# Optimization experiments

Measured on AMD Instinct MI355X. Metric: run time of the kernel, lower is better.

## Reference

```python
import jax, jax.numpy as jnp
import numpy as np
import math

VOCAB = 128
READ_DIM = 128
LOGIT_SCALE = 1.0 / 16.0
NUM_FF = 6
CARRY_DIM = 896
D_MODEL = CARRY_DIM + READ_DIM


def ste_sign(x):
    # forward of the STE sign: +-1, zero -> +1
    return jnp.where(x >= 0, 1.0, -1.0).astype(x.dtype)


def ste_round(x):
    return jnp.round(x)


def setup_inputs() -> dict:
    key = jax.random.key(0)
    k_tok, k_init, k_emb, k_ff, k_head, k_thr = jax.random.split(key, 6)
    tokens = jax.random.randint(k_tok, (64, 512), 0, VOCAB, dtype=jnp.int64) if jax.config.read('jax_enable_x64') else jax.random.randint(k_tok, (64, 512), 0, VOCAB, dtype=jnp.int32)
    initial_lat = jax.random.uniform(k_init, (D_MODEL,), minval=-1.0, maxval=1.0)
    embed_lat = jax.random.uniform(k_emb, (VOCAB, READ_DIM), minval=-1.0, maxval=1.0)
    ff_lat = jax.random.uniform(k_ff, (NUM_FF, D_MODEL, D_MODEL), minval=-1.0, maxval=1.0)
    head_lat = jax.random.uniform(k_head, (READ_DIM, VOCAB), minval=-1.0, maxval=1.0)
    ff_thresh_lat = jax.random.uniform(k_thr, (NUM_FF, D_MODEL), minval=-2.0, maxval=2.0)
    return {
        'tokens': tokens,
        'initial_lat': initial_lat,
        'embed_lat': embed_lat,
        'ff_lat': ff_lat,
        'head_lat': head_lat,
        'ff_thresh_lat': ff_thresh_lat,
    }


def reference(tokens, initial_lat, embed_lat, ff_lat, head_lat, ff_thresh_lat):
    B, T = tokens.shape
    num_ff = ff_lat.shape[0]
    d_model = initial_lat.shape[0]
    carry_dim = d_model - READ_DIM
    act_scale = math.sqrt(d_model)

    initial = ste_sign(initial_lat)          # [d_model]
    embed = ste_sign(embed_lat)              # [VOCAB, read_dim]
    ff = ste_sign(ff_lat)                    # [num_ff, d_model, d_model]
    head = ste_sign(head_lat)                # [read_dim, VOCAB]
    thr = ste_round(ff_thresh_lat)           # [num_ff, d_model]

    x0 = jnp.broadcast_to(initial[None, :], (B, d_model))

    def step(x, tok_t):
        # tok_t: [B]
        h = x
        for i in range(num_ff):
            pre = h @ ff[i]                  # [B, d_model]
            h = ste_sign((pre - thr[i]) / act_scale)
        carry = h[:, :carry_dim]
        read = h[:, carry_dim:]
        logits = read @ head * LOGIT_SCALE   # [B, VOCAB]
        logp = jax.nn.log_softmax(logits, axis=-1)
        loss_t = -jnp.mean(jnp.take_along_axis(logp, tok_t[:, None], axis=1))
        x_new = jnp.concatenate([carry, embed[tok_t]], axis=1)
        return x_new, loss_t

    _, losses = jax.lax.scan(step, x0, tokens.T)  # scan over T
    return jnp.mean(losses)
```

## Files before the change

### kernel.cpp

```cpp
#include <hip/hip_runtime.h>
#include <stdint.h>

typedef unsigned long long u64;
typedef uint32_t u32;

#define VOCAB 128
#define RD 128
#define DM 1024
#define NFF 6
#define BATCH 64
#define TSTEPS 512
#define NLOC 3
#define THR 256

#define OFF_EB    786432
#define OFF_HB    788480
#define OFF_LOSS  790528
#define OFF_XBUF  791040
#define OFF_MBUF  799232
#define OFF_FA    807424
#define OFF_FB    807680

__device__ __forceinline__ void wait_ge(const u32* f, u32 target) {
    while (__hip_atomic_load(f, __ATOMIC_ACQUIRE, __HIP_MEMORY_SCOPE_AGENT) < target)
        __builtin_amdgcn_s_sleep(1);
}

__global__ void pack_ff(const float* __restrict__ ff, u64* __restrict__ ffb) {
    int wid  = blockIdx.x * (blockDim.x >> 6) + (threadIdx.x >> 6);
    int lane = threadIdx.x & 63;
    int jt = wid & 15;
    int w  = (wid >> 4) & 15;
    int i  = wid >> 8;
    int j  = jt * 64 + lane;
    const float* src = ff + ((size_t)(i * DM) + w * 64) * DM + j;
    u64 word = 0;
#pragma unroll
    for (int b = 0; b < 64; ++b) {
        float v = src[(size_t)b * DM];
        word |= (u64)(v < 0.0f) << b;
    }
    ffb[((i * 16 + w) << 10) + j] = word;
}

__global__ void pack_small(const float* __restrict__ emb, const float* __restrict__ head,
                           u64* __restrict__ eb, u64* __restrict__ hb) {
    int tid = threadIdx.x;
    if (tid < 128) {
        int v = tid;
        for (int wd = 0; wd < 2; ++wd) {
            u64 word = 0;
            for (int l = 0; l < 64; ++l)
                word |= (u64)(emb[v * RD + wd * 64 + l] < 0.0f) << l;
            eb[v * 2 + wd] = word;
        }
    } else {
        int v = tid - 128;
        for (int wd = 0; wd < 2; ++wd) {
            u64 word = 0;
            for (int l = 0; l < 64; ++l)
                word |= (u64)(head[(wd * 64 + l) * VOCAB + v] < 0.0f) << l;
            hb[v * 2 + wd] = word;
        }
    }
}

#define PASS(P, L, EMIT) do {                                                   \
    const ulonglong2* hp_ = (const ulonglong2*)hx[P];                           \
    int a0_ = 0, a1_ = 0, a2_ = 0, a3_ = 0;                                     \
    _Pragma("unroll")                                                           \
    for (int q_ = 0; q_ < 8; ++q_) {                                            \
        ulonglong2 hv_ = hp_[q_];                   \
        a0_ += __popcll(hv_.x ^ fr[L][0][2*q_]) + __popcll(hv_.y ^ fr[L][0][2*q_+1]); \
        a1_ += __popcll(hv_.x ^ fr[L][1][2*q_]) + __popcll(hv_.y ^ fr[L][1][2*q_+1]); \
        a2_ += __popcll(hv_.x ^ fr[L][2][2*q_]) + __popcll(hv_.y ^ fr[L][2][2*q_+1]); \
        a3_ += __popcll(hv_.x ^ fr[L][3][2*q_]) + __popcll(hv_.y ^ fr[L][3][2*q_+1]); \
    }                                                                           \
    u64 m0_ = __ballot(a0_ >= cthr[L][0]);                                      \
    u64 m1_ = __ballot(a1_ >= cthr[L][1]);                                      \
    u64 m2_ = __ballot(a2_ >= cthr[L][2]);                                      \
    u64 m3_ = __ballot(a3_ >= cthr[L][3]);                                      \
    EMIT;                                                                       \
    __syncthreads();                                                            \
} while (0)

__global__ void
__attribute__((amdgpu_flat_work_group_size(256, 256), amdgpu_waves_per_eu(1, 1)))
brnn_pipe(const int* __restrict__ tokens,
          const float* __restrict__ initial_lat,
          const float* __restrict__ thr_lat,
          const u64* __restrict__ ffb,
          const u64* __restrict__ eb,
          const u64* __restrict__ hb,
          u64* __restrict__ xbuf, u64* __restrict__ mbuf,
          u32* __restrict__ fA, u32* __restrict__ fB,
          double* __restrict__ losses)
{
    const int blk  = blockIdx.x;
    const int role = blk >> 5;
    const int g    = blk & 31;
    const int tid  = threadIdx.x;
    const int lane = tid & 63;
    const int wv   = tid >> 6;

    __shared__ __align__(16) u64 hx[2][16];
    __shared__ u64 hbL[2 * VOCAB];

    const int lbase = role * NLOC;

    u64 fr[NLOC][4][16];
#pragma unroll
    for (int l = 0; l < NLOC; ++l)
#pragma unroll
        for (int c = 0; c < 4; ++c)
#pragma unroll
            for (int w = 0; w < 16; ++w)
                fr[l][c][w] = ffb[(((lbase + l) * 16 + w) << 10) + c * THR + tid];

    int cthr[NLOC][4];
#pragma unroll
    for (int l = 0; l < NLOC; ++l)
#pragma unroll
        for (int c = 0; c < 4; ++c) {
            int th = (int)rintf(thr_lat[(lbase + l) * DM + c * THR + tid]);
            cthr[l][c] = ((DM - th) >> 1) + 1;
        }

    if (role == 1 && tid < 2 * VOCAB) hbL[tid] = hb[tid];

    double lacc0 = 0.0, lacc1 = 0.0;
    const int r0 = 2 * g;

    if (role == 0) {
        for (int t = 0; t < TSTEPS; ++t) {
#pragma unroll
            for (int ri = 0; ri < 2; ++ri) {
                const int r = r0 + ri;
                if (t == 0) {
#pragma unroll
                    for (int c = 0; c < 4; ++c) {
                        u64 m = __ballot(initial_lat[c * THR + tid] < 0.0f);
                        if (lane == 0) hx[0][c * 4 + wv] = m;
                    }
                } else {
                    wait_ge(&fB[r], (u32)t);
                    if (wv == 0 && lane < 16) hx[0][lane] = xbuf[r * 16 + lane];
                }
                __syncthreads();
                PASS(0, 0, if (lane == 0) { hx[1][wv] = m0_; hx[1][4 + wv] = m1_;
                                            hx[1][8 + wv] = m2_; hx[1][12 + wv] = m3_; });
                PASS(1, 1, if (lane == 0) { hx[0][wv] = m0_; hx[0][4 + wv] = m1_;
                                            hx[0][8 + wv] = m2_; hx[0][12 + wv] = m3_; });
                PASS(0, 2, if (lane == 0) { mbuf[r * 16 + wv] = m0_;
                                            mbuf[r * 16 + 4 + wv] = m1_;
                                            mbuf[r * 16 + 8 + wv] = m2_;
                                            mbuf[r * 16 + 12 + wv] = m3_; });
                if (tid == 0)
                    __hip_atomic_store(&fA[r], (u32)(t + 1), __ATOMIC_RELEASE,
                                       __HIP_MEMORY_SCOPE_AGENT);
            }
        }
    } else {
        for (int t = 0; t < TSTEPS; ++t) {
#pragma unroll
            for (int ri = 0; ri < 2; ++ri) {
                const int r = r0 + ri;
                wait_ge(&fA[r], (u32)(t + 1));
                const int tok = tokens[r * TSTEPS + t];
                u64 enew = 0;
                if (wv == 0 && lane < 2) enew = eb[tok * 2 + lane];
                if (wv == 0 && lane < 16) hx[0][lane] = mbuf[r * 16 + lane];
                __syncthreads();
                PASS(0, 0, if (lane == 0) { hx[1][wv] = m0_; hx[1][4 + wv] = m1_;
                                            hx[1][8 + wv] = m2_; hx[1][12 + wv] = m3_; });
                PASS(1, 1, if (lane == 0) { hx[0][wv] = m0_; hx[0][4 + wv] = m1_;
                                            hx[0][8 + wv] = m2_; hx[0][12 + wv] = m3_; });
                PASS(0, 2, if (lane == 0) {
                        hx[1][wv] = m0_;      hx[1][4 + wv] = m1_;
                        hx[1][8 + wv] = m2_;  hx[1][12 + wv] = m3_;
                        xbuf[r * 16 + wv] = m0_;
                        xbuf[r * 16 + 4 + wv] = m1_;
                        xbuf[r * 16 + 8 + wv] = m2_;
                        if (wv < 2) xbuf[r * 16 + 12 + wv] = m3_; });
                if (wv == 0) {
                    u64 ra = hx[1][14], rb = hx[1][15];
                    u64 h0a = hbL[lane * 2 + 0],        h0b = hbL[lane * 2 + 1];
                    u64 h1a = hbL[(lane + 64) * 2 + 0], h1b = hbL[(lane + 64) * 2 + 1];
                    int d0 = 128 - 2 * (__popcll(ra ^ h0a) + __popcll(rb ^ h0b));
                    int d1 = 128 - 2 * (__popcll(ra ^ h1a) + __popcll(rb ^ h1b));
                    float l0 = (float)d0 * (1.0f / 16.0f);
                    float l1 = (float)d1 * (1.0f / 16.0f);
                    float mx = fmaxf(l0, l1);
#pragma unroll
                    for (int s = 32; s >= 1; s >>= 1) mx = fmaxf(mx, __shfl_xor(mx, s));
                    float se = __expf(l0 - mx) + __expf(l1 - mx);
#pragma unroll
                    for (int s = 32; s >= 1; s >>= 1) se += __shfl_xor(se, s);
                    int   tl   = tok & 63;
                    float la   = __shfl(l0, tl);
                    float lb_  = __shfl(l1, tl);
                    float ltok = (tok >> 6) ? lb_ : la;
                    double dl = (double)(mx + __logf(se) - ltok);
                    if (ri == 0) lacc0 += dl; else lacc1 += dl;
                    if (lane < 2) xbuf[r * 16 + 14 + lane] = enew;
                }
                __syncthreads();
                if (tid == 0)
                    __hip_atomic_store(&fB[r], (u32)(t + 1), __ATOMIC_RELEASE,
                                       __HIP_MEMORY_SCOPE_AGENT);
            }
        }
        if (tid == 0) { losses[r0] = lacc0; losses[r0 + 1] = lacc1; }
    }
}

__global__ void reduce_loss(const double* __restrict__ losses, float* __restrict__ out) {
    int lane = threadIdx.x;
    double v = losses[lane];
#pragma unroll
    for (int s = 32; s >= 1; s >>= 1) v += __shfl_down(v, s);
    if (lane == 0) out[0] = (float)(v * (1.0 / ((double)BATCH * (double)TSTEPS)));
}

extern "C" void kernel_launch(void* const* d_in, const int* in_sizes, int n_in,
                              void* d_out, int out_size, void* d_ws, size_t ws_size,
                              hipStream_t stream) {
    const int*   tokens  = (const int*)d_in[0];
    const float* initial = (const float*)d_in[1];
    const float* embed   = (const float*)d_in[2];
    const float* ff      = (const float*)d_in[3];
    const float* head    = (const float*)d_in[4];
    const float* thrl    = (const float*)d_in[5];

    char* ws = (char*)d_ws;
    u64*    ffb    = (u64*)ws;
    u64*    eb     = (u64*)(ws + OFF_EB);
    u64*    hb     = (u64*)(ws + OFF_HB);
    double* losses = (double*)(ws + OFF_LOSS);
    u64*    xbuf   = (u64*)(ws + OFF_XBUF);
    u64*    mbuf   = (u64*)(ws + OFF_MBUF);
    u32*    fAf    = (u32*)(ws + OFF_FA);
    u32*    fBf    = (u32*)(ws + OFF_FB);

    hipMemsetAsync(ws + OFF_FA, 0, 512, stream);

    pack_ff<<<384, 256, 0, stream>>>(ff, ffb);
    pack_small<<<1, 256, 0, stream>>>(embed, head, eb, hb);
    brnn_pipe<<<BATCH, THR, 0, stream>>>(tokens, initial, thrl, ffb, eb, hb,
                                         xbuf, mbuf, fAf, fBf, losses);
    reduce_loss<<<1, 64, 0, stream>>>(losses, (float*)d_out);
}
```

Baseline: 6.477 ms.

## Double block threads and move third layer's weights into LDS

Each pipeline block now runs 512 threads, so each thread owns 2 output columns per layer instead of 4. The first two layers' packed weights stay in registers and the third layer's weights are staged in shared memory and read during its pass. The aim is to cut the serial popcount work per thread along the recurrence's critical path by spreading it over more waves. The cost is extra LDS traffic in the third pass, more barrier participants, and a changed mapping of ballot words to the hx/mbuf/xbuf layout.

```diff
diff --git a/kernel.cpp b/kernel.cpp
--- a/kernel.cpp
+++ b/kernel.cpp
@@ -11,7 +11,7 @@
 #define BATCH 64
 #define TSTEPS 512
 #define NLOC 3
-#define THR 256
+#define THR 512
 
 #define OFF_EB    786432
 #define OFF_HB    788480
@@ -65,27 +65,40 @@
     }
 }
 
-#define PASS(P, L, EMIT) do {                                                   \
+#define REG_PASS(P, L, EMIT) do {                                               \
     const ulonglong2* hp_ = (const ulonglong2*)hx[P];                           \
-    int a0_ = 0, a1_ = 0, a2_ = 0, a3_ = 0;                                     \
+    int a0_ = 0, a1_ = 0;                                                       \
     _Pragma("unroll")                                                           \
     for (int q_ = 0; q_ < 8; ++q_) {                                            \
         ulonglong2 hv_ = hp_[q_];                   \
         a0_ += __popcll(hv_.x ^ fr[L][0][2*q_]) + __popcll(hv_.y ^ fr[L][0][2*q_+1]); \
         a1_ += __popcll(hv_.x ^ fr[L][1][2*q_]) + __popcll(hv_.y ^ fr[L][1][2*q_+1]); \
-        a2_ += __popcll(hv_.x ^ fr[L][2][2*q_]) + __popcll(hv_.y ^ fr[L][2][2*q_+1]); \
-        a3_ += __popcll(hv_.x ^ fr[L][3][2*q_]) + __popcll(hv_.y ^ fr[L][3][2*q_+1]); \
     }                                                                           \
     u64 m0_ = __ballot(a0_ >= cthr[L][0]);                                      \
     u64 m1_ = __ballot(a1_ >= cthr[L][1]);                                      \
-    u64 m2_ = __ballot(a2_ >= cthr[L][2]);                                      \
-    u64 m3_ = __ballot(a3_ >= cthr[L][3]);                                      \
     EMIT;                                                                       \
     __syncthreads();                                                            \
 } while (0)
 
+#define LDS_PASS(P, EMIT) do {                                                  \
+    const ulonglong2* hp_ = (const ulonglong2*)hx[P];                           \
+    int a0_ = 0, a1_ = 0;                                                       \
+    _Pragma("unroll")                                                           \
+    for (int q_ = 0; q_ < 8; ++q_) {                                            \
+        ulonglong2 hv_ = hp_[q_];                                               \
+        ulonglong2 w0_ = *(const ulonglong2*)wlds[q_][tid];                     \
+        ulonglong2 w1_ = *(const ulonglong2*)wlds[q_][512 + tid];               \
+        a0_ += __popcll(hv_.x ^ w0_.x) + __popcll(hv_.y ^ w0_.y);               \
+        a1_ += __popcll(hv_.x ^ w1_.x) + __popcll(hv_.y ^ w1_.y);               \
+    }                                                                           \
+    u64 m0_ = __ballot(a0_ >= cthr[2][0]);                                      \
+    u64 m1_ = __ballot(a1_ >= cthr[2][1]);                                      \
+    EMIT;                                                                       \
+    __syncthreads();                                                            \
+} while (0)
+
 __global__ void
-__attribute__((amdgpu_flat_work_group_size(256, 256), amdgpu_waves_per_eu(1, 1)))
+__attribute__((amdgpu_flat_work_group_size(THR, THR), amdgpu_waves_per_eu(1, 2)))
 brnn_pipe(const int* __restrict__ tokens,
           const float* __restrict__ initial_lat,
           const float* __restrict__ thr_lat,
@@ -103,25 +116,37 @@
     const int lane = tid & 63;
     const int wv   = tid >> 6;
 
+    __shared__ __align__(16) u64 wlds[8][1024][2];
     __shared__ __align__(16) u64 hx[2][16];
     __shared__ u64 hbL[2 * VOCAB];
 
     const int lbase = role * NLOC;
 
-    u64 fr[NLOC][4][16];
-#pragma unroll
-    for (int l = 0; l < NLOC; ++l)
-#pragma unroll
-        for (int c = 0; c < 4; ++c)
+#pragma unroll
+    for (int wp = 0; wp < 8; ++wp)
+#pragma unroll
+        for (int c = 0; c < 2; ++c) {
+            int j = c * THR + tid;
+            u64 lo = ffb[(((lbase + 2) * 16 + 2 * wp)     << 10) + j];
+            u64 hi = ffb[(((lbase + 2) * 16 + 2 * wp + 1) << 10) + j];
+            wlds[wp][j][0] = lo;
+            wlds[wp][j][1] = hi;
+        }
+
+    u64 fr[2][2][16];
+#pragma unroll
+    for (int l = 0; l < 2; ++l)
+#pragma unroll
+        for (int c = 0; c < 2; ++c)
 #pragma unroll
             for (int w = 0; w < 16; ++w)
                 fr[l][c][w] = ffb[(((lbase + l) * 16 + w) << 10) + c * THR + tid];
 
-    int cthr[NLOC][4];
+    int cthr[NLOC][2];
 #pragma unroll
     for (int l = 0; l < NLOC; ++l)
 #pragma unroll
-        for (int c = 0; c < 4; ++c) {
+        for (int c = 0; c < 2; ++c) {
             int th = (int)rintf(thr_lat[(lbase + l) * DM + c * THR + tid]);
             cthr[l][c] = ((DM - th) >> 1) + 1;
         }
@@ -138,23 +163,19 @@
                 const int r = r0 + ri;
                 if (t == 0) {
 #pragma unroll
-                    for (int c = 0; c < 4; ++c) {
+                    for (int c = 0; c < 2; ++c) {
                         u64 m = __ballot(initial_lat[c * THR + tid] < 0.0f);
-                        if (lane == 0) hx[0][c * 4 + wv] = m;
+                        if (lane == 0) hx[0][c * 8 + wv] = m;
                     }
                 } else {
                     wait_ge(&fB[r], (u32)t);
                     if (wv == 0 && lane < 16) hx[0][lane] = xbuf[r * 16 + lane];
                 }
                 __syncthreads();
-                PASS(0, 0, if (lane == 0) { hx[1][wv] = m0_; hx[1][4 + wv] = m1_;
-                                            hx[1][8 + wv] = m2_; hx[1][12 + wv] = m3_; });
-                PASS(1, 1, if (lane == 0) { hx[0][wv] = m0_; hx[0][4 + wv] = m1_;
-                                            hx[0][8 + wv] = m2_; hx[0][12 + wv] = m3_; });
-                PASS(0, 2, if (lane == 0) { mbuf[r * 16 + wv] = m0_;
-                                            mbuf[r * 16 + 4 + wv] = m1_;
-                                            mbuf[r * 16 + 8 + wv] = m2_;
-                                            mbuf[r * 16 + 12 + wv] = m3_; });
+                REG_PASS(0, 0, if (lane == 0) { hx[1][wv] = m0_; hx[1][8 + wv] = m1_; });
+                REG_PASS(1, 1, if (lane == 0) { hx[0][wv] = m0_; hx[0][8 + wv] = m1_; });
+                LDS_PASS(0,    if (lane == 0) { mbuf[r * 16 + wv] = m0_;
+                                                mbuf[r * 16 + 8 + wv] = m1_; });
                 if (tid == 0)
                     __hip_atomic_store(&fA[r], (u32)(t + 1), __ATOMIC_RELEASE,
                                        __HIP_MEMORY_SCOPE_AGENT);
@@ -171,17 +192,12 @@
                 if (wv == 0 && lane < 2) enew = eb[tok * 2 + lane];
                 if (wv == 0 && lane < 16) hx[0][lane] = mbuf[r * 16 + lane];
                 __syncthreads();
-                PASS(0, 0, if (lane == 0) { hx[1][wv] = m0_; hx[1][4 + wv] = m1_;
-                                            hx[1][8 + wv] = m2_; hx[1][12 + wv] = m3_; });
-                PASS(1, 1, if (lane == 0) { hx[0][wv] = m0_; hx[0][4 + wv] = m1_;
-                                            hx[0][8 + wv] = m2_; hx[0][12 + wv] = m3_; });
-                PASS(0, 2, if (lane == 0) {
-                        hx[1][wv] = m0_;      hx[1][4 + wv] = m1_;
-                        hx[1][8 + wv] = m2_;  hx[1][12 + wv] = m3_;
-                        xbuf[r * 16 + wv] = m0_;
-                        xbuf[r * 16 + 4 + wv] = m1_;
-                        xbuf[r * 16 + 8 + wv] = m2_;
-                        if (wv < 2) xbuf[r * 16 + 12 + wv] = m3_; });
+                REG_PASS(0, 0, if (lane == 0) { hx[1][wv] = m0_; hx[1][8 + wv] = m1_; });
+                REG_PASS(1, 1, if (lane == 0) { hx[0][wv] = m0_; hx[0][8 + wv] = m1_; });
+                LDS_PASS(0,    if (lane == 0) {
+                                   hx[1][wv] = m0_; hx[1][8 + wv] = m1_;
+                                   xbuf[r * 16 + wv] = m0_;
+                                   if (wv < 6) xbuf[r * 16 + 8 + wv] = m1_; });
                 if (wv == 0) {
                     u64 ra = hx[1][14], rb = hx[1][15];
                     u64 h0a = hbL[lane * 2 + 0],        h0b = hbL[lane * 2 + 1];
```

Result: slower. 7.967 ms (+23.0%).
